# Optimization experiments

Hardware: AMD Instinct MI355X
Metric: run time of the kernel (lower is better)

Reference implementation:

```python
import jax, jax.numpy as jnp
import numpy as np

N, DQ, T, H1 = 131072, 256, 4, 512

def setup_inputs() -> dict:
    key = jax.random.key(0)
    k_q, k_w0, k_b0, k_w1, k_z = jax.random.split(key, 5)
    return {
        "q": jax.random.normal(k_q, (N, DQ), dtype=jnp.float32),
        "Z": jax.random.randint(k_z, (N,), 0, T, dtype=jnp.int32),
        "W0": jax.random.normal(k_w0, (T, DQ, H1), dtype=jnp.float32) * (1.0 / np.sqrt(DQ)),
        "b0": jax.random.normal(k_b0, (T, H1), dtype=jnp.float32) * 0.01,
        "W1": jax.random.normal(k_w1, (T, H1), dtype=jnp.float32) * (1.0 / np.sqrt(H1)),
        "b1": jnp.zeros((), dtype=jnp.float32),
    }

def reference(q, Z, W0, b0, W1, b1):
    # Dense grouped-GEMM over all T types (T is small), then select per-atom
    # type result. Avoids materializing the per-atom [N, dq, h1] gathered
    # weight tensor that tf.gather would create.
    h_all = jnp.einsum('nd,tdh->nth', q, W0)              # [N, T, H1]
    h = jnp.take_along_axis(h_all, Z[:, None, None].astype(jnp.int32), axis=1)[:, 0, :]  # [N, H1]
    h = jnp.tanh(h + b0[Z])                               # hidden activations
    F = jnp.einsum('nh,nh->n', h, W1[Z]) + b1             # [N]
    return F
```

## Files before the change

### kernel.cpp

```cpp
#include <hip/hip_runtime.h>
#include <hip/hip_bf16.h>

#define N_ATOMS 131072
#define DQ 256
#define H1 512
#define NTYPES 4
#define TILE_M 64
#define NPAD (N_ATOMS + NTYPES * TILE_M)
#define MTILES ((N_ATOMS / TILE_M) + NTYPES)

typedef __bf16 bf16x8 __attribute__((ext_vector_type(8)));
typedef float f32x16 __attribute__((ext_vector_type(16)));

__device__ __forceinline__ unsigned short f2bf(float f) {
  unsigned int u = __builtin_bit_cast(unsigned int, f);
  u += 0x7fffu + ((u >> 16) & 1u);
  return (unsigned short)(u >> 16);
}

__device__ __forceinline__ float fast_tanh(float x) {
  float e = __expf(2.0f * x);
  return 1.0f - 2.0f * __builtin_amdgcn_rcpf(e + 1.0f);
}

__global__ __launch_bounds__(256) void prep_kernel(
    const float* __restrict__ W0, const int* __restrict__ Z,
    unsigned short* __restrict__ W0s, int* __restrict__ perm,
    int* __restrict__ blockcounts)
{
  const int b = blockIdx.x, tid = threadIdx.x;
  const int gid = b * 256 + tid;

  for (int i = gid; i < NPAD; i += 512 * 256) perm[i] = -1;

  if (gid < NTYPES * (DQ / 8) * H1) {
    const int n  = gid & (H1 - 1);
    const int kg = (gid >> 9) & 31;
    const int t  = gid >> 14;
    const float* src = W0 + ((size_t)(t * DQ + kg * 8) * H1 + n);
    unsigned short o[8];
#pragma unroll
    for (int j = 0; j < 8; ++j) o[j] = f2bf(src[(size_t)j * H1]);
    uint4 v;
    v.x = (unsigned)o[0] | ((unsigned)o[1] << 16);
    v.y = (unsigned)o[2] | ((unsigned)o[3] << 16);
    v.z = (unsigned)o[4] | ((unsigned)o[5] << 16);
    v.w = (unsigned)o[6] | ((unsigned)o[7] << 16);
    ((uint4*)W0s)[gid] = v;
  }

  __shared__ int lc[NTYPES];
  if (tid < NTYPES) lc[tid] = 0;
  __syncthreads();
  atomicAdd(&lc[Z[gid]], 1);
  __syncthreads();
  if (tid < NTYPES) blockcounts[b * NTYPES + tid] = lc[tid];
}

__global__ __launch_bounds__(256) void scan_kernel(
    const int* __restrict__ blockcounts, int* __restrict__ padded_off,
    int* __restrict__ cursors)
{
  __shared__ int sums[NTYPES];
  const int tid = threadIdx.x;
  if (tid < NTYPES) sums[tid] = 0;
  __syncthreads();
  const int t = tid & 3;
  int acc = 0;
  for (int b = tid >> 2; b < 512; b += 64) acc += blockcounts[b * 4 + t];
  atomicAdd(&sums[t], acc);
  __syncthreads();
  if (tid == 0) {
    int off = 0;
#pragma unroll
    for (int i = 0; i < NTYPES; ++i) {
      padded_off[i] = off;
      cursors[i] = off;
      off += (sums[i] + TILE_M - 1) & ~(TILE_M - 1);
    }
    padded_off[NTYPES] = off;
  }
}

__global__ __launch_bounds__(256) void scatter_kernel(
    const int* __restrict__ Z, int* __restrict__ cursors, int* __restrict__ perm)
{
  __shared__ int lc[NTYPES], lbase[NTYPES];
  const int tid = threadIdx.x;
  const int gid = blockIdx.x * 256 + tid;
  if (tid < NTYPES) lc[tid] = 0;
  __syncthreads();
  const int t  = Z[gid];
  const int my = atomicAdd(&lc[t], 1);
  __syncthreads();
  if (tid < NTYPES) lbase[tid] = lc[tid] ? atomicAdd(&cursors[tid], lc[tid]) : 0;
  __syncthreads();
  perm[lbase[t] + my] = gid;
}

__global__ __launch_bounds__(256, 2) void gemm_kernel(
    const float* __restrict__ q, const int* __restrict__ perm,
    const int* __restrict__ padded_off, const unsigned short* __restrict__ W0s,
    const float* __restrict__ b0, const float* __restrict__ W1,
    const float* __restrict__ b1p, float* __restrict__ out)
{
  __shared__ unsigned short Alds[(DQ / 8) * TILE_M * 8];
  __shared__ float Fws[4][TILE_M];

  const int gr0 = blockIdx.x * TILE_M;
  if (gr0 >= padded_off[NTYPES]) return;
  int t = 0;
#pragma unroll
  for (int i = 1; i < NTYPES; ++i) t += (gr0 >= padded_off[i]) ? 1 : 0;

  const int tid = threadIdx.x;

  {
    const int row = tid >> 2, c4 = tid & 3;
    const int atom = perm[gr0 + row];
    const float* qrow = q + (size_t)(atom < 0 ? 0 : atom) * DQ;
#pragma unroll
    for (int i = 0; i < 16; ++i) {
      const int k = c4 * 64 + i * 4;
      float4 v = make_float4(0.f, 0.f, 0.f, 0.f);
      if (atom >= 0) v = *(const float4*)(qrow + k);
      ushort4 o;
      o.x = f2bf(v.x); o.y = f2bf(v.y); o.z = f2bf(v.z); o.w = f2bf(v.w);
      *(ushort4*)&Alds[((k >> 3) * TILE_M + row) * 8 + (k & 7)] = o;
    }
  }
  __syncthreads();

  const int l = tid & 63, w = tid >> 6;
  const int half = l >> 5, ln = l & 31;

  f32x16 acc[2][4];
#pragma unroll
  for (int mt = 0; mt < 2; ++mt)
#pragma unroll
    for (int nt = 0; nt < 4; ++nt) acc[mt][nt] = (f32x16)0.0f;

  const unsigned short* Bt = W0s + (size_t)t * (DQ * H1);
  const unsigned short* Bbase = Bt + (size_t)(w * 128 + ln) * 8;

#pragma unroll 4
  for (int step = 0; step < 16; ++step) {
    const int kg = 2 * step + half;
    const bf16x8 a0 = *(const bf16x8*)&Alds[(kg * TILE_M + ln) * 8];
    const bf16x8 a1 = *(const bf16x8*)&Alds[(kg * TILE_M + 32 + ln) * 8];
    const unsigned short* bp = Bbase + (size_t)kg * (H1 * 8);
    const bf16x8 b0f = *(const bf16x8*)(bp);
    const bf16x8 b1f = *(const bf16x8*)(bp + 32 * 8);
    const bf16x8 b2f = *(const bf16x8*)(bp + 64 * 8);
    const bf16x8 b3f = *(const bf16x8*)(bp + 96 * 8);
    acc[0][0] = __builtin_amdgcn_mfma_f32_32x32x16_bf16(a0, b0f, acc[0][0], 0, 0, 0);
    acc[1][0] = __builtin_amdgcn_mfma_f32_32x32x16_bf16(a1, b0f, acc[1][0], 0, 0, 0);
    acc[0][1] = __builtin_amdgcn_mfma_f32_32x32x16_bf16(a0, b1f, acc[0][1], 0, 0, 0);
    acc[1][1] = __builtin_amdgcn_mfma_f32_32x32x16_bf16(a1, b1f, acc[1][1], 0, 0, 0);
    acc[0][2] = __builtin_amdgcn_mfma_f32_32x32x16_bf16(a0, b2f, acc[0][2], 0, 0, 0);
    acc[1][2] = __builtin_amdgcn_mfma_f32_32x32x16_bf16(a1, b2f, acc[1][2], 0, 0, 0);
    acc[0][3] = __builtin_amdgcn_mfma_f32_32x32x16_bf16(a0, b3f, acc[0][3], 0, 0, 0);
    acc[1][3] = __builtin_amdgcn_mfma_f32_32x32x16_bf16(a1, b3f, acc[1][3], 0, 0, 0);
  }

  float b0v[4], w1v[4];
#pragma unroll
  for (int nt = 0; nt < 4; ++nt) {
    const int c = w * 128 + nt * 32 + ln;
    b0v[nt] = b0[t * H1 + c];
    w1v[nt] = W1[t * H1 + c];
  }
#pragma unroll
  for (int mt = 0; mt < 2; ++mt) {
#pragma unroll
    for (int r = 0; r < 16; ++r) {
      float s = 0.f;
#pragma unroll
      for (int nt = 0; nt < 4; ++nt)
        s += w1v[nt] * fast_tanh(acc[mt][nt][r] + b0v[nt]);
      s += __shfl_xor(s, 1);
      s += __shfl_xor(s, 2);
      s += __shfl_xor(s, 4);
      s += __shfl_xor(s, 8);
      s += __shfl_xor(s, 16);
      if (ln == 0)
        Fws[w][mt * 32 + (r & 3) + 8 * (r >> 2) + 4 * half] = s;
    }
  }
  __syncthreads();

  if (tid < TILE_M) {
    const int atom = perm[gr0 + tid];
    if (atom >= 0)
      out[atom] = Fws[0][tid] + Fws[1][tid] + Fws[2][tid] + Fws[3][tid] + b1p[0];
  }
}

extern "C" void kernel_launch(void* const* d_in, const int* in_sizes, int n_in,
                              void* d_out, int out_size, void* d_ws, size_t ws_size,
                              hipStream_t stream) {
  const float* q  = (const float*)d_in[0];
  const int*   Z  = (const int*)d_in[1];
  const float* W0 = (const float*)d_in[2];
  const float* b0 = (const float*)d_in[3];
  const float* W1 = (const float*)d_in[4];
  const float* b1 = (const float*)d_in[5];
  float* out = (float*)d_out;

  char* ws = (char*)d_ws;
  int* blockcounts = (int*)(ws);
  int* padded_off  = (int*)(ws + 8192);
  int* cursors     = (int*)(ws + 8192 + 32);
  int* perm        = (int*)(ws + 8192 + 64);
  unsigned short* W0s = (unsigned short*)(ws + 8192 + 64 + (size_t)NPAD * 4);

  hipLaunchKernelGGL(prep_kernel,    dim3(512),    dim3(256), 0, stream, W0, Z, W0s, perm, blockcounts);
  hipLaunchKernelGGL(scan_kernel,    dim3(1),      dim3(256), 0, stream, blockcounts, padded_off, cursors);
  hipLaunchKernelGGL(scatter_kernel, dim3(512),    dim3(256), 0, stream, Z, cursors, perm);
  hipLaunchKernelGGL(gemm_kernel,    dim3(MTILES), dim3(256), 0, stream, q, perm, padded_off, W0s, b0, W1, b1, out);
}
```

Before: 282.0 us.

## Make grouped GEMM persistent per type with register-resident weights and double-buffered tiles

The GEMM kernel becomes persistent: 64 blocks per type loop over that type's 64-row tiles. Each of the 8 waves keeps its 64-column slice of the bf16 weights in registers for the whole run, and the next q tile is prefetched into a second LDS buffer while the current one is computed. The W0 conversion moves into its own kernel, which transposes through shared memory so global reads and writes are coalesced. This removes repeated weight reloads from global memory and overlaps q loads with MFMA work, at the cost of high register pressure (64 VGPRs per lane for B) and load imbalance when type counts differ.

Measured after the change: 320.5 us. +13.6%, slower.

```diff
diff --git a/kernel.cpp b/kernel.cpp
--- a/kernel.cpp
+++ b/kernel.cpp
@@ -7,7 +7,7 @@
 #define NTYPES 4
 #define TILE_M 64
 #define NPAD (N_ATOMS + NTYPES * TILE_M)
-#define MTILES ((N_ATOMS / TILE_M) + NTYPES)
+#define BLOCKS_PER_TYPE 64
 
 typedef __bf16 bf16x8 __attribute__((ext_vector_type(8)));
 typedef float f32x16 __attribute__((ext_vector_type(16)));
@@ -17,44 +17,54 @@
   u += 0x7fffu + ((u >> 16) & 1u);
   return (unsigned short)(u >> 16);
 }
-
+__device__ __forceinline__ unsigned int pack2(float a, float b) {
+  return (unsigned int)f2bf(a) | ((unsigned int)f2bf(b) << 16);
+}
 __device__ __forceinline__ float fast_tanh(float x) {
   float e = __expf(2.0f * x);
   return 1.0f - 2.0f * __builtin_amdgcn_rcpf(e + 1.0f);
 }
 
-__global__ __launch_bounds__(256) void prep_kernel(
-    const float* __restrict__ W0, const int* __restrict__ Z,
-    unsigned short* __restrict__ W0s, int* __restrict__ perm,
+__global__ __launch_bounds__(256) void hist_kernel(
+    const int* __restrict__ Z, int* __restrict__ perm,
     int* __restrict__ blockcounts)
 {
   const int b = blockIdx.x, tid = threadIdx.x;
   const int gid = b * 256 + tid;
-
   for (int i = gid; i < NPAD; i += 512 * 256) perm[i] = -1;
-
-  if (gid < NTYPES * (DQ / 8) * H1) {
-    const int n  = gid & (H1 - 1);
-    const int kg = (gid >> 9) & 31;
-    const int t  = gid >> 14;
-    const float* src = W0 + ((size_t)(t * DQ + kg * 8) * H1 + n);
-    unsigned short o[8];
-#pragma unroll
-    for (int j = 0; j < 8; ++j) o[j] = f2bf(src[(size_t)j * H1]);
-    uint4 v;
-    v.x = (unsigned)o[0] | ((unsigned)o[1] << 16);
-    v.y = (unsigned)o[2] | ((unsigned)o[3] << 16);
-    v.z = (unsigned)o[4] | ((unsigned)o[5] << 16);
-    v.w = (unsigned)o[6] | ((unsigned)o[7] << 16);
-    ((uint4*)W0s)[gid] = v;
-  }
-
   __shared__ int lc[NTYPES];
   if (tid < NTYPES) lc[tid] = 0;
   __syncthreads();
   atomicAdd(&lc[Z[gid]], 1);
   __syncthreads();
   if (tid < NTYPES) blockcounts[b * NTYPES + tid] = lc[tid];
+}
+
+__global__ __launch_bounds__(256) void w0s_kernel(
+    const float* __restrict__ W0, unsigned short* __restrict__ W0s)
+{
+  __shared__ __align__(16) unsigned short S[64][72];
+  const int b = blockIdx.x;
+  const int nb = b & 7, kb = (b >> 3) & 3, t = b >> 5;
+  const int tid = threadIdx.x;
+  const int kl = tid >> 4, nl = (tid & 15) * 4;
+#pragma unroll
+  for (int r = 0; r < 4; ++r) {
+    const int k = r * 16 + kl;
+    const float4 v = *(const float4*)&W0[((size_t)(t * DQ + kb * 64 + k)) * H1 + nb * 64 + nl];
+    S[nl + 0][k] = f2bf(v.x);
+    S[nl + 1][k] = f2bf(v.y);
+    S[nl + 2][k] = f2bf(v.z);
+    S[nl + 3][k] = f2bf(v.w);
+  }
+  __syncthreads();
+#pragma unroll
+  for (int r = 0; r < 2; ++r) {
+    const int c = r * 256 + tid;
+    const int n = c & 63, kg2l = c >> 6;
+    const uint4 v = *(const uint4*)&S[n][kg2l * 8];
+    ((uint4*)W0s)[(size_t)(t * 32 + kb * 8 + kg2l) * H1 + nb * 64 + n] = v;
+  }
 }
 
 __global__ __launch_bounds__(256) void scan_kernel(
@@ -98,101 +108,138 @@
   perm[lbase[t] + my] = gid;
 }
 
-__global__ __launch_bounds__(256, 2) void gemm_kernel(
+__device__ __forceinline__ void load_tile(const float* __restrict__ q,
+    const int* __restrict__ perm, int row0, int w, int l, float4 ld[8]) {
+  int atom = perm[row0 + l];
+  if (atom < 0) atom = 0;
+  const float* src = q + (size_t)atom * DQ + w * 32;
+#pragma unroll
+  for (int i = 0; i < 8; ++i) ld[i] = *(const float4*)(src + i * 4);
+}
+
+__device__ __forceinline__ void store_tile(unsigned short* Abuf, int w, int l,
+                                           const float4 ld[8]) {
+#pragma unroll
+  for (int i = 0; i < 4; ++i) {
+    uint4 v;
+    v.x = pack2(ld[2 * i].x, ld[2 * i].y);
+    v.y = pack2(ld[2 * i].z, ld[2 * i].w);
+    v.z = pack2(ld[2 * i + 1].x, ld[2 * i + 1].y);
+    v.w = pack2(ld[2 * i + 1].z, ld[2 * i + 1].w);
+    *(uint4*)&Abuf[((w * 4 + i) * 64 + l) * 8] = v;
+  }
+}
+
+__global__ __launch_bounds__(512, 2) void gemm_kernel(
     const float* __restrict__ q, const int* __restrict__ perm,
     const int* __restrict__ padded_off, const unsigned short* __restrict__ W0s,
     const float* __restrict__ b0, const float* __restrict__ W1,
     const float* __restrict__ b1p, float* __restrict__ out)
 {
-  __shared__ unsigned short Alds[(DQ / 8) * TILE_M * 8];
-  __shared__ float Fws[4][TILE_M];
-
-  const int gr0 = blockIdx.x * TILE_M;
-  if (gr0 >= padded_off[NTYPES]) return;
-  int t = 0;
-#pragma unroll
-  for (int i = 1; i < NTYPES; ++i) t += (gr0 >= padded_off[i]) ? 1 : 0;
-
-  const int tid = threadIdx.x;
-
-  {
-    const int row = tid >> 2, c4 = tid & 3;
-    const int atom = perm[gr0 + row];
-    const float* qrow = q + (size_t)(atom < 0 ? 0 : atom) * DQ;
-#pragma unroll
-    for (int i = 0; i < 16; ++i) {
-      const int k = c4 * 64 + i * 4;
-      float4 v = make_float4(0.f, 0.f, 0.f, 0.f);
-      if (atom >= 0) v = *(const float4*)(qrow + k);
-      ushort4 o;
-      o.x = f2bf(v.x); o.y = f2bf(v.y); o.z = f2bf(v.z); o.w = f2bf(v.w);
-      *(ushort4*)&Alds[((k >> 3) * TILE_M + row) * 8 + (k & 7)] = o;
-    }
-  }
-  __syncthreads();
-
-  const int l = tid & 63, w = tid >> 6;
+  __shared__ __align__(16) unsigned short A[2][32 * 64 * 8];
+  __shared__ float Fws[8][64];
+
+  const int tid = threadIdx.x;
+  const int w = tid >> 6, l = tid & 63;
   const int half = l >> 5, ln = l & 31;
 
-  f32x16 acc[2][4];
-#pragma unroll
-  for (int mt = 0; mt < 2; ++mt)
-#pragma unroll
-    for (int nt = 0; nt < 4; ++nt) acc[mt][nt] = (f32x16)0.0f;
-
-  const unsigned short* Bt = W0s + (size_t)t * (DQ * H1);
-  const unsigned short* Bbase = Bt + (size_t)(w * 128 + ln) * 8;
-
-#pragma unroll 4
-  for (int step = 0; step < 16; ++step) {
-    const int kg = 2 * step + half;
-    const bf16x8 a0 = *(const bf16x8*)&Alds[(kg * TILE_M + ln) * 8];
-    const bf16x8 a1 = *(const bf16x8*)&Alds[(kg * TILE_M + 32 + ln) * 8];
-    const unsigned short* bp = Bbase + (size_t)kg * (H1 * 8);
-    const bf16x8 b0f = *(const bf16x8*)(bp);
-    const bf16x8 b1f = *(const bf16x8*)(bp + 32 * 8);
-    const bf16x8 b2f = *(const bf16x8*)(bp + 64 * 8);
-    const bf16x8 b3f = *(const bf16x8*)(bp + 96 * 8);
-    acc[0][0] = __builtin_amdgcn_mfma_f32_32x32x16_bf16(a0, b0f, acc[0][0], 0, 0, 0);
-    acc[1][0] = __builtin_amdgcn_mfma_f32_32x32x16_bf16(a1, b0f, acc[1][0], 0, 0, 0);
-    acc[0][1] = __builtin_amdgcn_mfma_f32_32x32x16_bf16(a0, b1f, acc[0][1], 0, 0, 0);
-    acc[1][1] = __builtin_amdgcn_mfma_f32_32x32x16_bf16(a1, b1f, acc[1][1], 0, 0, 0);
-    acc[0][2] = __builtin_amdgcn_mfma_f32_32x32x16_bf16(a0, b2f, acc[0][2], 0, 0, 0);
-    acc[1][2] = __builtin_amdgcn_mfma_f32_32x32x16_bf16(a1, b2f, acc[1][2], 0, 0, 0);
-    acc[0][3] = __builtin_amdgcn_mfma_f32_32x32x16_bf16(a0, b3f, acc[0][3], 0, 0, 0);
-    acc[1][3] = __builtin_amdgcn_mfma_f32_32x32x16_bf16(a1, b3f, acc[1][3], 0, 0, 0);
-  }
-
-  float b0v[4], w1v[4];
-#pragma unroll
-  for (int nt = 0; nt < 4; ++nt) {
-    const int c = w * 128 + nt * 32 + ln;
+  const int t = blockIdx.x >> 6;
+  const int bslot = blockIdx.x & 63;
+  const int seg0 = padded_off[t];
+  const int ntiles = (padded_off[t + 1] - seg0) >> 6;
+  if (bslot >= ntiles) return;
+
+  const int colbase = w * 64;
+
+  float b0v[2], w1v[2];
+#pragma unroll
+  for (int nt = 0; nt < 2; ++nt) {
+    const int c = colbase + nt * 32 + ln;
     b0v[nt] = b0[t * H1 + c];
     w1v[nt] = W1[t * H1 + c];
   }
-#pragma unroll
-  for (int mt = 0; mt < 2; ++mt) {
-#pragma unroll
-    for (int r = 0; r < 16; ++r) {
-      float s = 0.f;
-#pragma unroll
-      for (int nt = 0; nt < 4; ++nt)
-        s += w1v[nt] * fast_tanh(acc[mt][nt][r] + b0v[nt]);
-      s += __shfl_xor(s, 1);
-      s += __shfl_xor(s, 2);
-      s += __shfl_xor(s, 4);
-      s += __shfl_xor(s, 8);
-      s += __shfl_xor(s, 16);
-      if (ln == 0)
-        Fws[w][mt * 32 + (r & 3) + 8 * (r >> 2) + 4 * half] = s;
-    }
-  }
-  __syncthreads();
-
-  if (tid < TILE_M) {
-    const int atom = perm[gr0 + tid];
-    if (atom >= 0)
-      out[atom] = Fws[0][tid] + Fws[1][tid] + Fws[2][tid] + Fws[3][tid] + b1p[0];
+  const float b1 = b1p[0];
+
+  const unsigned short* Bt = W0s + (size_t)t * (DQ * H1);
+  bf16x8 Bf[16][2];
+#pragma unroll
+  for (int ks = 0; ks < 16; ++ks) {
+    const int kg2 = ks * 2 + half;
+#pragma unroll
+    for (int nt = 0; nt < 2; ++nt)
+      Bf[ks][nt] = *(const bf16x8*)(Bt + ((size_t)kg2 * H1 + colbase + nt * 32 + ln) * 8);
+  }
+
+  int j = bslot;
+  int row0 = seg0 + (j << 6);
+  {
+    float4 ld[8];
+    load_tile(q, perm, row0, w, l, ld);
+    store_tile(A[0], w, l, ld);
+  }
+  __syncthreads();
+  int p = 0;
+
+  for (;;) {
+    const int jn = j + BLOCKS_PER_TYPE;
+    const bool have_next = jn < ntiles;
+    const int row0n = seg0 + (jn << 6);
+
+    float4 ld[8];
+    if (have_next) load_tile(q, perm, row0n, w, l, ld);
+
+    const unsigned short* Acur = A[p];
+    f32x16 acc[2][2];
+#pragma unroll
+    for (int mt = 0; mt < 2; ++mt)
+#pragma unroll
+      for (int nt = 0; nt < 2; ++nt) acc[mt][nt] = (f32x16)0.0f;
+
+#pragma unroll
+    for (int ks = 0; ks < 16; ++ks) {
+      const int kg2 = ks * 2 + half;
+      const bf16x8 a0 = *(const bf16x8*)&Acur[(kg2 * 64 + ln) * 8];
+      const bf16x8 a1 = *(const bf16x8*)&Acur[(kg2 * 64 + 32 + ln) * 8];
+      acc[0][0] = __builtin_amdgcn_mfma_f32_32x32x16_bf16(a0, Bf[ks][0], acc[0][0], 0, 0, 0);
+      acc[1][0] = __builtin_amdgcn_mfma_f32_32x32x16_bf16(a1, Bf[ks][0], acc[1][0], 0, 0, 0);
+      acc[0][1] = __builtin_amdgcn_mfma_f32_32x32x16_bf16(a0, Bf[ks][1], acc[0][1], 0, 0, 0);
+      acc[1][1] = __builtin_amdgcn_mfma_f32_32x32x16_bf16(a1, Bf[ks][1], acc[1][1], 0, 0, 0);
+    }
+
+#pragma unroll
+    for (int mt = 0; mt < 2; ++mt) {
+#pragma unroll
+      for (int r = 0; r < 16; ++r) {
+        float s = w1v[0] * fast_tanh(acc[mt][0][r] + b0v[0])
+                + w1v[1] * fast_tanh(acc[mt][1][r] + b0v[1]);
+        s += __shfl_xor(s, 1);
+        s += __shfl_xor(s, 2);
+        s += __shfl_xor(s, 4);
+        s += __shfl_xor(s, 8);
+        s += __shfl_xor(s, 16);
+        if (ln == 0)
+          Fws[w][mt * 32 + (r & 3) + 8 * (r >> 2) + 4 * half] = s;
+      }
+    }
+    __syncthreads();
+
+    if (tid < TILE_M) {
+      const int atom = perm[row0 + tid];
+      if (atom >= 0) {
+        float f = b1;
+#pragma unroll
+        for (int ww = 0; ww < 8; ++ww) f += Fws[ww][tid];
+        out[atom] = f;
+      }
+    }
+
+    if (!have_next) break;
+
+    store_tile(A[1 - p], w, l, ld);
+    __syncthreads();
+    p ^= 1;
+    j = jn;
+    row0 = row0n;
   }
 }
 
@@ -214,8 +261,10 @@
   int* perm        = (int*)(ws + 8192 + 64);
   unsigned short* W0s = (unsigned short*)(ws + 8192 + 64 + (size_t)NPAD * 4);
 
-  hipLaunchKernelGGL(prep_kernel,    dim3(512),    dim3(256), 0, stream, W0, Z, W0s, perm, blockcounts);
-  hipLaunchKernelGGL(scan_kernel,    dim3(1),      dim3(256), 0, stream, blockcounts, padded_off, cursors);
-  hipLaunchKernelGGL(scatter_kernel, dim3(512),    dim3(256), 0, stream, Z, cursors, perm);
-  hipLaunchKernelGGL(gemm_kernel,    dim3(MTILES), dim3(256), 0, stream, q, perm, padded_off, W0s, b0, W1, b1, out);
-}
+  hipLaunchKernelGGL(hist_kernel,    dim3(512), dim3(256), 0, stream, Z, perm, blockcounts);
+  hipLaunchKernelGGL(w0s_kernel,     dim3(128), dim3(256), 0, stream, W0, W0s);
+  hipLaunchKernelGGL(scan_kernel,    dim3(1),   dim3(256), 0, stream, blockcounts, padded_off, cursors);
+  hipLaunchKernelGGL(scatter_kernel, dim3(512), dim3(256), 0, stream, Z, cursors, perm);
+  hipLaunchKernelGGL(gemm_kernel,    dim3(NTYPES * BLOCKS_PER_TYPE), dim3(512), 0, stream,
+                     q, perm, padded_off, W0s, b0, W1, b1, out);
+}
```
